# Kernel optimization log

Hardware: AMD Instinct MI355X
Metric: run time of the kernel (lower is better)

## Reference

```python
import jax, jax.numpy as jnp
import numpy as np

N_NODES = 50000
N_EDGES = 800000
F = 64
EPS = 1e-5


def batchnorm(x, gamma, beta):
    # training-mode BatchNorm1d: batch mean, biased variance
    mu = jnp.mean(x, axis=0)
    var = jnp.mean((x - mu) ** 2, axis=0)
    return gamma * (x - mu) * jax.lax.rsqrt(var + EPS) + beta


def setup_inputs() -> dict:
    key = jax.random.key(0)
    ks = jax.random.split(key, 10)
    s = 1.0 / np.sqrt(3 * F)
    return {
        "node_feats": jax.random.normal(ks[0], (N_NODES, F), jnp.float32),
        "edge_feats": jax.random.normal(ks[1], (N_EDGES, F), jnp.float32),
        "src": jax.random.randint(ks[2], (N_EDGES,), 0, N_NODES, jnp.int32),
        "dst": jax.random.randint(ks[3], (N_EDGES,), 0, N_NODES, jnp.int32),
        "W_mlpt": jax.random.uniform(ks[4], (3 * F, F), jnp.float32, -s, s),
        "b_mlpt": jnp.zeros((F,), jnp.float32),
        "g_mlpt": jnp.ones((F,), jnp.float32),
        "be_mlpt": jnp.zeros((F,), jnp.float32),
        "W_gate": jax.random.uniform(ks[5], (3 * F, F), jnp.float32, -s, s),
        "b_gate": jnp.zeros((F,), jnp.float32),
        "g_gate": jnp.ones((F,), jnp.float32),
        "be_gate": jnp.zeros((F,), jnp.float32),
        "g_node": jnp.ones((F,), jnp.float32),
        "be_node": jnp.zeros((F,), jnp.float32),
    }


def reference(node_feats, edge_feats, src, dst,
              W_mlpt, b_mlpt, g_mlpt, be_mlpt,
              W_gate, b_gate, g_gate, be_gate,
              g_node, be_node):
    # edge-wise gather + concat: [E, 3F]
    h_cat = jnp.concatenate(
        [node_feats[src], node_feats[dst], edge_feats], axis=1)
    # two small MLPs: Linear + BN + activation (dropout p=0)
    h_mlpt = jax.nn.sigmoid(batchnorm(h_cat @ W_mlpt + b_mlpt, g_mlpt, be_mlpt))
    h_gate = jax.nn.softplus(batchnorm(h_cat @ W_gate + b_gate, g_gate, be_gate))
    h_upd = h_mlpt * h_gate  # [E, F]
    # scatter-sum messages onto destination nodes
    agg = jax.ops.segment_sum(h_upd, dst, num_segments=N_NODES)  # [N, F]
    node_out = jax.nn.sigmoid(batchnorm(agg, g_node, be_node) + node_feats)
    return (node_out, edge_feats)
```

## Files before the change

kernel.cpp:

```cpp
#include <hip/hip_runtime.h>

#define E_TOT   800000
#define NN      50000
#define FF      64

typedef __attribute__((ext_vector_type(8))) short  short8;
typedef __attribute__((ext_vector_type(4))) float  f32x4;
typedef __attribute__((ext_vector_type(4))) unsigned int u32x4;

__device__ __forceinline__ unsigned short f2bf(float f) {
  union { float f; unsigned int u; } v; v.f = f;
  unsigned int r = v.u + 0x7fffu + ((v.u >> 16) & 1u);
  return (unsigned short)(r >> 16);
}

__device__ __forceinline__ unsigned int pkbf(float a, float b) {
  unsigned int r;
  asm("v_cvt_pk_bf16_f32 %0, %1, %2" : "=v"(r) : "v"(a), "v"(b));
  return r;
}

__device__ __forceinline__ void atomic_pk_bf16(unsigned short* p, unsigned int v) {
  asm volatile("global_atomic_pk_add_bf16 %0, %1, off" :: "v"(p), "v"(v) : "memory");
}

__device__ __forceinline__ float bflo(unsigned int u) { return __uint_as_float(u << 16); }
__device__ __forceinline__ float bfhi(unsigned int u) { return __uint_as_float(u & 0xffff0000u); }

__device__ __forceinline__ float sigmoidf_(float x) {
  return 1.f / (1.f + __expf(-x));
}

__device__ __forceinline__ f32x4 nt_load_f4(const float* p) {
  return __builtin_nontemporal_load((const f32x4*)p);
}
__device__ __forceinline__ void nt_store_f4(float* p, f32x4 v) {
  __builtin_nontemporal_store(v, (f32x4*)p);
}
__device__ __forceinline__ u32x4 nt_load_u4(const unsigned int* p) {
  return __builtin_nontemporal_load((const u32x4*)p);
}
__device__ __forceinline__ void nt_store_u4(unsigned int* p, u32x4 v) {
  __builtin_nontemporal_store(v, (u32x4*)p);
}

__global__ void cvt_node(const float2* __restrict__ nf, unsigned int* __restrict__ nb) {
  int i = blockIdx.x * 256 + threadIdx.x;
  float2 v = nf[i];
  nb[i] = pkbf(v.x, v.y);
}

__global__ void pack_w(const float* __restrict__ Wm, const float* __restrict__ Wg,
                       unsigned short* __restrict__ Wp) {
  int t = blockIdx.x * 256 + threadIdx.x;
  if (t >= 3072) return;
  int lane = t & 63;
  int kk   = (t >> 6) % 6;
  int mnt  = t / 384;
  const float* W = (mnt >> 2) ? Wg : Wm;
  int nt  = mnt & 3;
  int col = nt * 16 + (lane & 15);
  int kb  = kk * 32 + (lane >> 4) * 8;
  #pragma unroll
  for (int j = 0; j < 8; ++j)
    Wp[t * 8 + j] = f2bf(W[(kb + j) * 64 + col]);
}

template <int NB>
__global__ __launch_bounds__(256, 5)
void edge_gemm(const float* __restrict__ nodef, const unsigned short* __restrict__ nodeb,
               const float* __restrict__ edgef,
               const int* __restrict__ src, const int* __restrict__ dst,
               const unsigned short* __restrict__ Wp,
               float* __restrict__ stats,
               unsigned int* __restrict__ Yw,
               float* __restrict__ outE, int write_copy)
{
  __shared__ unsigned short sh[64 * 200];
  __shared__ float red[4 * 256];

  const int tid = threadIdx.x;
  const int e0  = blockIdx.x * 64;
  const int row = tid >> 2;
  const int cq  = tid & 3;

  const int s = src[e0 + row], d = dst[e0 + row];
  unsigned short* rowp = &sh[row * 200];

  if constexpr (NB) {
    const unsigned int* qs = (const unsigned int*)(nodeb + (size_t)s * 64) + cq * 8;
    const unsigned int* qd = (const unsigned int*)(nodeb + (size_t)d * 64) + cq * 8;
    u32x4 s0 = *(const u32x4*)qs,       s1 = *(const u32x4*)(qs + 4);
    u32x4 d0 = *(const u32x4*)qd,       d1 = *(const u32x4*)(qd + 4);
    *(u32x4*)(rowp + cq * 16)          = s0;
    *(u32x4*)(rowp + cq * 16 + 8)      = s1;
    *(u32x4*)(rowp + 64 + cq * 16)     = d0;
    *(u32x4*)(rowp + 64 + cq * 16 + 8) = d1;
  } else {
    const float* ps = nodef + (size_t)s * 64 + cq * 4;
    const float* pd = nodef + (size_t)d * 64 + cq * 4;
    #pragma unroll
    for (int it = 0; it < 4; ++it) {
      float4 v0 = *(const float4*)(ps + it * 16);
      float4 v1 = *(const float4*)(pd + it * 16);
      *(uint2*)(rowp + cq * 4 + it * 16)      = make_uint2(pkbf(v0.x, v0.y), pkbf(v0.z, v0.w));
      *(uint2*)(rowp + 64 + cq * 4 + it * 16) = make_uint2(pkbf(v1.x, v1.y), pkbf(v1.z, v1.w));
    }
  }

  const float* pe = edgef + (size_t)(e0 + row) * 64 + cq * 4;
  f32x4 ev[4];
  #pragma unroll
  for (int it = 0; it < 4; ++it) {
    ev[it] = nt_load_f4(pe + it * 16);
    *(uint2*)(rowp + 128 + cq * 4 + it * 16) =
        make_uint2(pkbf(ev[it].x, ev[it].y), pkbf(ev[it].z, ev[it].w));
  }
  if (write_copy) {
    float* op = outE + (size_t)(e0 + row) * 64 + cq * 4;
    #pragma unroll
    for (int it = 0; it < 4; ++it)
      nt_store_f4(op + it * 16, ev[it]);
  }

  asm volatile("s_waitcnt lgkmcnt(0)" ::: "memory");

  const int w = tid >> 6, lane = tid & 63;
  f32x4 acc[8] = {};
  const unsigned short* abase = &sh[(w * 16 + (lane & 15)) * 200 + (lane >> 4) * 8];
  const short8* wp = (const short8*)Wp;

  #pragma unroll
  for (int kk = 0; kk < 6; ++kk) {
    short8 a = *(const short8*)(abase + kk * 32);
    #pragma unroll
    for (int nt = 0; nt < 8; ++nt) {
      short8 b = wp[(nt * 6 + kk) * 64 + lane];
      acc[nt] = __builtin_amdgcn_mfma_f32_16x16x32_bf16(a, b, acc[nt], 0, 0, 0);
    }
  }

  unsigned int* yb = Yw + ((((size_t)blockIdx.x * 4 + w) * 4) * 64 + lane) * 4;
  #pragma unroll
  for (int ntp = 0; ntp < 4; ++ntp) {
    u32x4 q;
    q.x = pkbf(acc[2 * ntp][0],     acc[2 * ntp][1]);
    q.y = pkbf(acc[2 * ntp][2],     acc[2 * ntp][3]);
    q.z = pkbf(acc[2 * ntp + 1][0], acc[2 * ntp + 1][1]);
    q.w = pkbf(acc[2 * ntp + 1][2], acc[2 * ntp + 1][3]);
    nt_store_u4(yb + ntp * 64 * 4, q);
  }

  #pragma unroll
  for (int nt = 0; nt < 8; ++nt) {
    float sv = acc[nt][0] + acc[nt][1] + acc[nt][2] + acc[nt][3];
    float qv = acc[nt][0] * acc[nt][0] + acc[nt][1] * acc[nt][1] +
               acc[nt][2] * acc[nt][2] + acc[nt][3] * acc[nt][3];
    sv += __shfl_xor(sv, 16); sv += __shfl_xor(sv, 32);
    qv += __shfl_xor(qv, 16); qv += __shfl_xor(qv, 32);
    if ((lane >> 4) == 0) {
      red[w * 256 + nt * 16 + lane]       = sv;
      red[w * 256 + 128 + nt * 16 + lane] = qv;
    }
  }
  __syncthreads();
  float v = red[tid] + red[256 + tid] + red[512 + tid] + red[768 + tid];
  atomicAdd(&stats[(blockIdx.x & 63) * 256 + tid], v);
}

__global__ void finalize_edge(const float* __restrict__ stats,
                              const float* __restrict__ g_m, const float* __restrict__ be_m,
                              const float* __restrict__ g_g, const float* __restrict__ be_g,
                              float* __restrict__ coef) {
  int c = threadIdx.x;
  float s = 0.f, q = 0.f;
  for (int sl = 0; sl < 64; ++sl) { s += stats[sl * 256 + c]; q += stats[sl * 256 + 128 + c]; }
  float mu  = s * (1.f / E_TOT);
  float var = fmaxf(q * (1.f / E_TOT) - mu * mu, 0.f);
  float g   = (c < 64) ? g_m[c]  : g_g[c - 64];
  float be  = (c < 64) ? be_m[c] : be_g[c - 64];
  float a   = g * rsqrtf(var + 1e-5f);
  coef[c]       = a;
  coef[128 + c] = be - mu * a;
}

__global__ __launch_bounds__(256)
void edge_apply(const unsigned int* __restrict__ Yw, const int* __restrict__ dst,
                const float* __restrict__ coef,
                unsigned short* __restrict__ aggb)
{
  const int tid = threadIdx.x;
  const int w = tid >> 6, lane = tid & 63;
  const int e0 = blockIdx.x * 64;
  const int r0 = w * 16 + ((lane >> 4) << 2);
  const int4 dn = *(const int4*)&dst[e0 + r0];
  const int colb = lane & 15;
  const int par  = colb & 1;

  const unsigned int* yb = Yw + ((((size_t)blockIdx.x * 4 + w) * 4) * 64 + lane) * 4;
  u32x4 qm0 = nt_load_u4(yb);
  u32x4 qm1 = nt_load_u4(yb + 64 * 4);
  u32x4 qg0 = nt_load_u4(yb + 128 * 4);
  u32x4 qg1 = nt_load_u4(yb + 192 * 4);
  const unsigned int um[8] = {qm0.x, qm0.y, qm0.z, qm0.w, qm1.x, qm1.y, qm1.z, qm1.w};
  const unsigned int ug[8] = {qg0.x, qg0.y, qg0.z, qg0.w, qg1.x, qg1.y, qg1.z, qg1.w};
  const int dr[4] = {dn.x, dn.y, dn.z, dn.w};

  #pragma unroll
  for (int ntm = 0; ntm < 4; ++ntm) {
    const int col = ntm * 16 + colb;
    const float am = coef[col],      cm = coef[128 + col];
    const float ag = coef[64 + col], cg = coef[192 + col];
    float hv[4];
    #pragma unroll
    for (int p = 0; p < 2; ++p) {
      unsigned int m = um[ntm * 2 + p], g = ug[ntm * 2 + p];
      #pragma unroll
      for (int h = 0; h < 2; ++h) {
        float mv = h ? bfhi(m) : bflo(m);
        float gv = h ? bfhi(g) : bflo(g);
        float ym = fmaf(mv, am, cm);
        float yg = fmaf(gv, ag, cg);
        float sig = sigmoidf_(ym);
        float sp  = (yg > 20.f) ? yg : __logf(1.f + __expf(yg));
        hv[2 * p + h] = sig * sp;
      }
    }
    float pv[4];
    #pragma unroll
    for (int rr = 0; rr < 4; ++rr) pv[rr] = __shfl_xor(hv[rr], 1);
    const int colp = ntm * 16 + (colb & ~1);
    #pragma unroll
    for (int rr = 0; rr < 2; ++rr) {
      int rx = par * 2 + rr;
      float lo = par ? pv[rx] : hv[rx];
      float hi = par ? hv[rx] : pv[rx];
      atomic_pk_bf16(&aggb[(size_t)dr[rx] * 64 + colp], pkbf(lo, hi));
    }
  }
}

__global__ void node_stats(const unsigned int* __restrict__ aggu, float* __restrict__ nstats) {
  __shared__ float rs0[256], rq0[256], rs1[256], rq1[256];
  int tid = threadIdx.x;
  int cp = tid & 31;
  float s0 = 0.f, q0 = 0.f, s1 = 0.f, q1 = 0.f;
  for (int r = blockIdx.x * 8 + (tid >> 5); r < NN; r += gridDim.x * 8) {
    unsigned int u = aggu[r * 32 + cp];
    float v0 = bflo(u), v1 = bfhi(u);
    s0 += v0; q0 += v0 * v0; s1 += v1; q1 += v1 * v1;
  }
  rs0[tid] = s0; rq0[tid] = q0; rs1[tid] = s1; rq1[tid] = q1;
  __syncthreads();
  if (tid < 32) {
    s0 = 0.f; q0 = 0.f; s1 = 0.f; q1 = 0.f;
    #pragma unroll
    for (int k = 0; k < 8; ++k) {
      s0 += rs0[tid + 32 * k]; q0 += rq0[tid + 32 * k];
      s1 += rs1[tid + 32 * k]; q1 += rq1[tid + 32 * k];
    }
    int slot = blockIdx.x & 31;
    atomicAdd(&nstats[slot * 128 + 2 * tid],      s0);
    atomicAdd(&nstats[slot * 128 + 2 * tid + 1],  s1);
    atomicAdd(&nstats[slot * 128 + 64 + 2 * tid],     q0);
    atomicAdd(&nstats[slot * 128 + 64 + 2 * tid + 1], q1);
  }
}

__global__ void finalize_node(const float* __restrict__ nstats,
                              const float* __restrict__ g_n, const float* __restrict__ be_n,
                              float* __restrict__ coefn) {
  int c = threadIdx.x;
  float s = 0.f, q = 0.f;
  for (int sl = 0; sl < 32; ++sl) { s += nstats[sl * 128 + c]; q += nstats[sl * 128 + 64 + c]; }
  float mu  = s * (1.f / NN);
  float var = fmaxf(q * (1.f / NN) - mu * mu, 0.f);
  float a   = g_n[c] * rsqrtf(var + 1e-5f);
  coefn[c]      = a;
  coefn[64 + c] = be_n[c] - mu * a;
}

__global__ void node_out_k(float* __restrict__ out, const unsigned int* __restrict__ aggu,
                           const float* __restrict__ nodef, const float* __restrict__ coefn) {
  int i  = blockIdx.x * 256 + threadIdx.x;
  int cb = (i & 15) * 4;
  uint2  u  = ((const uint2*)aggu)[i];
  float4 nf = ((const float4*)nodef)[i];
  float4 r;
  r.x = sigmoidf_(coefn[cb + 0] * bflo(u.x) + coefn[64 + cb + 0] + nf.x);
  r.y = sigmoidf_(coefn[cb + 1] * bfhi(u.x) + coefn[64 + cb + 1] + nf.y);
  r.z = sigmoidf_(coefn[cb + 2] * bflo(u.y) + coefn[64 + cb + 2] + nf.z);
  r.w = sigmoidf_(coefn[cb + 3] * bfhi(u.y) + coefn[64 + cb + 3] + nf.w);
  ((float4*)out)[i] = r;
}

extern "C" void kernel_launch(void* const* d_in, const int* in_sizes, int n_in,
                              void* d_out, int out_size, void* d_ws, size_t ws_size,
                              hipStream_t stream) {
  const float* nodef = (const float*)d_in[0];
  const float* edgef = (const float*)d_in[1];
  const int*   src   = (const int*)d_in[2];
  const int*   dst   = (const int*)d_in[3];
  const float* W_m   = (const float*)d_in[4];
  const float* g_m   = (const float*)d_in[6];
  const float* be_m  = (const float*)d_in[7];
  const float* W_g   = (const float*)d_in[8];
  const float* g_g   = (const float*)d_in[10];
  const float* be_g  = (const float*)d_in[11];
  const float* g_n   = (const float*)d_in[12];
  const float* be_n  = (const float*)d_in[13];

  float* out  = (float*)d_out;
  float* outE = out + (size_t)NN * FF;

  char* ws = (char*)d_ws;
  unsigned short* aggb = (unsigned short*)ws;
  float* stats  = (float*)(ws + 0x640000);
  float* coef   = (float*)(ws + 0x650000);
  float* nstats = (float*)(ws + 0x651000);
  float* coefn  = (float*)(ws + 0x655000);
  unsigned short* Wp = (unsigned short*)(ws + 0x656000);

  const size_t y_bytes = (size_t)E_TOT * 128 * 2;
  const int y_in_ws = (ws_size >= (size_t)0x700000 + y_bytes);
  unsigned int* Yw = y_in_ws ? (unsigned int*)(ws + 0x700000) : (unsigned int*)outE;

  const size_t nb_off = y_in_ws ? ((size_t)0x700000 + y_bytes) : (size_t)0x700000;
  const int use_nb = (ws_size >= nb_off + (size_t)NN * FF * 2);
  unsigned short* nodeb = (unsigned short*)(ws + nb_off);

  hipMemsetAsync(aggb, 0, (size_t)NN * FF * 2, stream);
  hipMemsetAsync(stats, 0, 0x15200, stream);

  pack_w<<<12, 256, 0, stream>>>(W_m, W_g, Wp);
  if (use_nb) {
    cvt_node<<<NN * 32 / 256, 256, 0, stream>>>((const float2*)nodef, (unsigned int*)nodeb);
    edge_gemm<1><<<E_TOT / 64, 256, 0, stream>>>(nodef, nodeb, edgef, src, dst, Wp,
                                                 stats, Yw, outE, y_in_ws);
  } else {
    edge_gemm<0><<<E_TOT / 64, 256, 0, stream>>>(nodef, nodeb, edgef, src, dst, Wp,
                                                 stats, Yw, outE, y_in_ws);
  }
  finalize_edge<<<1, 128, 0, stream>>>(stats, g_m, be_m, g_g, be_g, coef);
  edge_apply<<<E_TOT / 64, 256, 0, stream>>>(Yw, dst, coef, aggb);
  if (!y_in_ws) {
    hipMemcpyAsync(outE, edgef, (size_t)E_TOT * FF * sizeof(float),
                   hipMemcpyDeviceToDevice, stream);
  }
  node_stats<<<512, 256, 0, stream>>>((const unsigned int*)aggb, nstats);
  finalize_node<<<1, 64, 0, stream>>>(nstats, g_n, be_n, coefn);
  node_out_k<<<NN * FF / 4 / 256, 256, 0, stream>>>(out, (const unsigned int*)aggb,
                                                    nodef, coefn);
}
```

Measured before the change: 380.6 us.

## Replace bf16 atomic scatter with CSR-sorted node-centric segmented sum

Builds a CSR index of edges grouped by destination node: a histogram of dst, a single-block scan and an atomic fill of edge ids. A new node-parallel kernel gathers each node's edge rows, applies the BN, sigmoid and softplus transform, and accumulates in fp32 registers. This replaces tens of millions of packed bf16 global atomics with a few million int atomics plus random row gathers. Edge GEMM output is rewritten through shared memory into a row-major per-edge layout so each edge's row can be fetched contiguously. The extra passes and scratch arrays are placed in the output buffer before it is overwritten, and the single-block scan adds serial latency.

```diff
diff --git a/kernel.cpp b/kernel.cpp
--- a/kernel.cpp
+++ b/kernel.cpp
@@ -18,10 +18,6 @@
   unsigned int r;
   asm("v_cvt_pk_bf16_f32 %0, %1, %2" : "=v"(r) : "v"(a), "v"(b));
   return r;
-}
-
-__device__ __forceinline__ void atomic_pk_bf16(unsigned short* p, unsigned int v) {
-  asm volatile("global_atomic_pk_add_bf16 %0, %1, off" :: "v"(p), "v"(v) : "memory");
 }
 
 __device__ __forceinline__ float bflo(unsigned int u) { return __uint_as_float(u << 16); }
@@ -66,6 +62,51 @@
     Wp[t * 8 + j] = f2bf(W[(kb + j) * 64 + col]);
 }
 
+__global__ void hist_k(const int* __restrict__ dst, int* __restrict__ counts) {
+  int e = blockIdx.x * 256 + threadIdx.x;
+  if (e < E_TOT) atomicAdd(&counts[dst[e]], 1);
+}
+
+__global__ __launch_bounds__(1024)
+void scan_k(const int* __restrict__ counts, int* __restrict__ offs, int* __restrict__ cursor) {
+  __shared__ int wsum[16];
+  const int t = threadIdx.x;
+  const int CH = 49;
+  int lo = t * CH, hi = min(lo + CH, NN);
+  if (lo > NN) lo = NN;
+  int s = 0;
+  for (int i = lo; i < hi; ++i) s += counts[i];
+  int lane = t & 63, w = t >> 6;
+  int v = s;
+  #pragma unroll
+  for (int dlt = 1; dlt < 64; dlt <<= 1) {
+    int u = __shfl_up(v, dlt);
+    if (lane >= dlt) v += u;
+  }
+  if (lane == 63) wsum[w] = v;
+  __syncthreads();
+  if (t == 0) {
+    int a = 0;
+    for (int i = 0; i < 16; ++i) { int c = wsum[i]; wsum[i] = a; a += c; }
+  }
+  __syncthreads();
+  int run = v - s + wsum[w];
+  for (int i = lo; i < hi; ++i) {
+    int c = counts[i];
+    offs[i] = run; cursor[i] = run;
+    run += c;
+  }
+}
+
+__global__ void fill_k(const int* __restrict__ dst, int* __restrict__ cursor,
+                       int* __restrict__ eid) {
+  int e = blockIdx.x * 256 + threadIdx.x;
+  if (e < E_TOT) {
+    int p = atomicAdd(&cursor[dst[e]], 1);
+    eid[p] = e;
+  }
+}
+
 template <int NB>
 __global__ __launch_bounds__(256, 5)
 void edge_gemm(const float* __restrict__ nodef, const unsigned short* __restrict__ nodeb,
@@ -73,7 +114,7 @@
                const int* __restrict__ src, const int* __restrict__ dst,
                const unsigned short* __restrict__ Wp,
                float* __restrict__ stats,
-               unsigned int* __restrict__ Yw,
+               unsigned int* __restrict__ Y,
                float* __restrict__ outE, int write_copy)
 {
   __shared__ unsigned short sh[64 * 200];
@@ -140,15 +181,21 @@
     }
   }
 
-  unsigned int* yb = Yw + ((((size_t)blockIdx.x * 4 + w) * 4) * 64 + lane) * 4;
-  #pragma unroll
-  for (int ntp = 0; ntp < 4; ++ntp) {
-    u32x4 q;
-    q.x = pkbf(acc[2 * ntp][0],     acc[2 * ntp][1]);
-    q.y = pkbf(acc[2 * ntp][2],     acc[2 * ntp][3]);
-    q.z = pkbf(acc[2 * ntp + 1][0], acc[2 * ntp + 1][1]);
-    q.w = pkbf(acc[2 * ntp + 1][2], acc[2 * ntp + 1][3]);
-    nt_store_u4(yb + ntp * 64 * 4, q);
+  asm volatile("s_waitcnt lgkmcnt(0)" ::: "memory");
+
+  unsigned int* shu = (unsigned int*)sh;
+  const int colb = lane & 15, rq = lane >> 4, par = colb & 1;
+  #pragma unroll
+  for (int nt = 0; nt < 8; ++nt) {
+    float hv0 = acc[nt][0], hv1 = acc[nt][1], hv2 = acc[nt][2], hv3 = acc[nt][3];
+    float pv0 = __shfl_xor(hv0, 1), pv1 = __shfl_xor(hv1, 1);
+    float pv2 = __shfl_xor(hv2, 1), pv3 = __shfl_xor(hv3, 1);
+    float loA = par ? pv2 : hv0,  hiA = par ? hv2 : pv0;
+    float loB = par ? pv3 : hv1,  hiB = par ? hv3 : pv1;
+    int r0 = rq * 4 + par * 2;
+    int ci = nt * 8 + (colb >> 1);
+    shu[(w * 16 + r0)     * 100 + ci] = pkbf(loA, hiA);
+    shu[(w * 16 + r0 + 1) * 100 + ci] = pkbf(loB, hiB);
   }
 
   #pragma unroll
@@ -164,6 +211,15 @@
     }
   }
   __syncthreads();
+
+  #pragma unroll
+  for (int k2 = 0; k2 < 4; ++k2) {
+    int k  = tid + k2 * 256;
+    int rw = k >> 4, part = k & 15;
+    u32x4 v = *(const u32x4*)&shu[rw * 100 + part * 4];
+    nt_store_u4(Y + (size_t)(e0 + rw) * 64 + part * 4, v);
+  }
+
   float v = red[tid] + red[256 + tid] + red[512 + tid] + red[768 + tid];
   atomicAdd(&stats[(blockIdx.x & 63) * 256 + tid], v);
 }
@@ -185,58 +241,67 @@
 }
 
 __global__ __launch_bounds__(256)
-void edge_apply(const unsigned int* __restrict__ Yw, const int* __restrict__ dst,
-                const float* __restrict__ coef,
-                unsigned short* __restrict__ aggb)
+void node_sum2(const unsigned int* __restrict__ Yu, const int* __restrict__ eid,
+               const int* __restrict__ offs, const int* __restrict__ counts,
+               const float* __restrict__ coef, unsigned int* __restrict__ aggu)
 {
   const int tid = threadIdx.x;
   const int w = tid >> 6, lane = tid & 63;
-  const int e0 = blockIdx.x * 64;
-  const int r0 = w * 16 + ((lane >> 4) << 2);
-  const int4 dn = *(const int4*)&dst[e0 + r0];
-  const int colb = lane & 15;
-  const int par  = colb & 1;
-
-  const unsigned int* yb = Yw + ((((size_t)blockIdx.x * 4 + w) * 4) * 64 + lane) * 4;
-  u32x4 qm0 = nt_load_u4(yb);
-  u32x4 qm1 = nt_load_u4(yb + 64 * 4);
-  u32x4 qg0 = nt_load_u4(yb + 128 * 4);
-  u32x4 qg1 = nt_load_u4(yb + 192 * 4);
-  const unsigned int um[8] = {qm0.x, qm0.y, qm0.z, qm0.w, qm1.x, qm1.y, qm1.z, qm1.w};
-  const unsigned int ug[8] = {qg0.x, qg0.y, qg0.z, qg0.w, qg1.x, qg1.y, qg1.z, qg1.w};
-  const int dr[4] = {dn.x, dn.y, dn.z, dn.w};
-
-  #pragma unroll
-  for (int ntm = 0; ntm < 4; ++ntm) {
-    const int col = ntm * 16 + colb;
-    const float am = coef[col],      cm = coef[128 + col];
-    const float ag = coef[64 + col], cg = coef[192 + col];
-    float hv[4];
+  const int n = blockIdx.x * 4 + w;
+  const int x = lane & 15, grp = lane >> 4;
+  const bool isg = x >= 8;
+  const int cb = (x & 7) * 8;
+
+  float A[8], C[8];
+  #pragma unroll
+  for (int k = 0; k < 8; ++k) {
+    A[k] = coef[(isg ? 64 : 0) + cb + k];
+    C[k] = coef[128 + (isg ? 64 : 0) + cb + k];
+  }
+
+  const int st = offs[n], deg = counts[n];
+  float a[8] = {};
+
+  for (int base = 0; base < deg; base += 16) {
     #pragma unroll
-    for (int p = 0; p < 2; ++p) {
-      unsigned int m = um[ntm * 2 + p], g = ug[ntm * 2 + p];
+    for (int i = 0; i < 4; ++i) {
+      int p = base + i * 4 + grp;
+      bool ok = p < deg;
+      int e = eid[st + (ok ? p : 0)];
+      u32x4 y = nt_load_u4(Yu + (size_t)e * 64 + x * 4);
+      float r[8];
       #pragma unroll
-      for (int h = 0; h < 2; ++h) {
-        float mv = h ? bfhi(m) : bflo(m);
-        float gv = h ? bfhi(g) : bflo(g);
-        float ym = fmaf(mv, am, cm);
-        float yg = fmaf(gv, ag, cg);
-        float sig = sigmoidf_(ym);
-        float sp  = (yg > 20.f) ? yg : __logf(1.f + __expf(yg));
-        hv[2 * p + h] = sig * sp;
+      for (int j = 0; j < 4; ++j) {
+        unsigned int u = y[j];
+        float v0 = fmaf(bflo(u), A[2 * j],     C[2 * j]);
+        float v1 = fmaf(bfhi(u), A[2 * j + 1], C[2 * j + 1]);
+        if (isg) {
+          r[2 * j]     = (v0 > 20.f) ? v0 : __logf(1.f + __expf(v0));
+          r[2 * j + 1] = (v1 > 20.f) ? v1 : __logf(1.f + __expf(v1));
+        } else {
+          r[2 * j]     = 1.f / (1.f + __expf(-v0));
+          r[2 * j + 1] = 1.f / (1.f + __expf(-v1));
+        }
+      }
+      #pragma unroll
+      for (int k = 0; k < 8; ++k) {
+        float pr = __shfl_xor(r[k], 8);
+        float h = r[k] * pr;
+        a[k] += ok ? h : 0.f;
       }
     }
-    float pv[4];
-    #pragma unroll
-    for (int rr = 0; rr < 4; ++rr) pv[rr] = __shfl_xor(hv[rr], 1);
-    const int colp = ntm * 16 + (colb & ~1);
-    #pragma unroll
-    for (int rr = 0; rr < 2; ++rr) {
-      int rx = par * 2 + rr;
-      float lo = par ? pv[rx] : hv[rx];
-      float hi = par ? hv[rx] : pv[rx];
-      atomic_pk_bf16(&aggb[(size_t)dr[rx] * 64 + colp], pkbf(lo, hi));
-    }
+  }
+
+  #pragma unroll
+  for (int k = 0; k < 8; ++k) {
+    a[k] += __shfl_xor(a[k], 16);
+    a[k] += __shfl_xor(a[k], 32);
+  }
+  if (lane < 8) {
+    u32x4 o;
+    o.x = pkbf(a[0], a[1]); o.y = pkbf(a[2], a[3]);
+    o.z = pkbf(a[4], a[5]); o.w = pkbf(a[6], a[7]);
+    *(u32x4*)(aggu + (size_t)n * 32 + lane * 4) = o;
   }
 }
 
@@ -313,6 +378,12 @@
   float* out  = (float*)d_out;
   float* outE = out + (size_t)NN * FF;
 
+  char* od = (char*)d_out;
+  int* counts = (int*)(od + 0x000000);
+  int* offs   = (int*)(od + 0x040000);
+  int* cursor = (int*)(od + 0x080000);
+  int* eid    = (int*)(od + 0x0C0000);
+
   char* ws = (char*)d_ws;
   unsigned short* aggb = (unsigned short*)ws;
   float* stats  = (float*)(ws + 0x640000);
@@ -321,9 +392,9 @@
   float* coefn  = (float*)(ws + 0x655000);
   unsigned short* Wp = (unsigned short*)(ws + 0x656000);
 
-  const size_t y_bytes = (size_t)E_TOT * 128 * 2;
+  const size_t y_bytes = (size_t)E_TOT * 64 * 4;
   const int y_in_ws = (ws_size >= (size_t)0x700000 + y_bytes);
-  unsigned int* Yw = y_in_ws ? (unsigned int*)(ws + 0x700000) : (unsigned int*)outE;
+  unsigned int* Y = y_in_ws ? (unsigned int*)(ws + 0x700000) : (unsigned int*)outE;
 
   const size_t nb_off = y_in_ws ? ((size_t)0x700000 + y_bytes) : (size_t)0x700000;
   const int use_nb = (ws_size >= nb_off + (size_t)NN * FF * 2);
@@ -331,18 +402,22 @@
 
   hipMemsetAsync(aggb, 0, (size_t)NN * FF * 2, stream);
   hipMemsetAsync(stats, 0, 0x15200, stream);
+  hipMemsetAsync(counts, 0, NN * sizeof(int), stream);
 
   pack_w<<<12, 256, 0, stream>>>(W_m, W_g, Wp);
+  hist_k<<<(E_TOT + 255) / 256, 256, 0, stream>>>(dst, counts);
   if (use_nb) {
     cvt_node<<<NN * 32 / 256, 256, 0, stream>>>((const float2*)nodef, (unsigned int*)nodeb);
     edge_gemm<1><<<E_TOT / 64, 256, 0, stream>>>(nodef, nodeb, edgef, src, dst, Wp,
-                                                 stats, Yw, outE, y_in_ws);
+                                                 stats, Y, outE, y_in_ws);
   } else {
     edge_gemm<0><<<E_TOT / 64, 256, 0, stream>>>(nodef, nodeb, edgef, src, dst, Wp,
-                                                 stats, Yw, outE, y_in_ws);
-  }
+                                                 stats, Y, outE, y_in_ws);
+  }
+  scan_k<<<1, 1024, 0, stream>>>(counts, offs, cursor);
   finalize_edge<<<1, 128, 0, stream>>>(stats, g_m, be_m, g_g, be_g, coef);
-  edge_apply<<<E_TOT / 64, 256, 0, stream>>>(Yw, dst, coef, aggb);
+  fill_k<<<(E_TOT + 255) / 256, 256, 0, stream>>>(dst, cursor, eid);
+  node_sum2<<<NN / 4, 256, 0, stream>>>(Y, eid, offs, counts, coef, (unsigned int*)aggb);
   if (!y_in_ws) {
     hipMemcpyAsync(outE, edgef, (size_t)E_TOT * FF * sizeof(float),
                    hipMemcpyDeviceToDevice, stream);
```

Result: slower. 602.7 us (+58.4%).
